# Kernel tuning notes

Measured on AMD Instinct MI355X. Metric: run time of the kernel, lower is better.

The kernel has to match this reference:

```python
import jax, jax.numpy as jnp
import numpy as np

B, N, D, R, H, E = 4, 8192, 16, 32, 64, 262144


def _linear_init(key, fan_in, fan_out):
    return jax.random.normal(key, (fan_in, fan_out), jnp.float32) * (1.0 / np.sqrt(fan_in))


def setup_inputs() -> dict:
    key = jax.random.key(0)
    ks = jax.random.split(key, 8)
    particles = jax.random.normal(ks[0], (B, N, D), jnp.float32)
    senders = jax.random.randint(ks[1], (E,), 0, N, dtype=jnp.int32)
    receivers = jax.random.randint(ks[2], (E,), 0, N, dtype=jnp.int32)
    # relation_encoder: Linear(2D->H), ReLU, Linear(H->R), ReLU
    W1 = _linear_init(ks[3], 2 * D, H)
    b1 = jnp.zeros((H,), jnp.float32)
    W2 = _linear_init(ks[4], H, R)
    b2 = jnp.zeros((R,), jnp.float32)
    # dynamics_fn: Linear(D+R->H), ReLU, Linear(H->D)
    W3 = _linear_init(ks[5], D + R, H)
    b3 = jnp.zeros((H,), jnp.float32)
    W4 = _linear_init(ks[6], H, D)
    b4 = jnp.zeros((D,), jnp.float32)
    return {"particles": particles, "senders": senders, "receivers": receivers,
            "W1": W1, "b1": b1, "W2": W2, "b2": b2,
            "W3": W3, "b3": b3, "W4": W4, "b4": b4}


def reference(particles, senders, receivers, W1, b1, W2, b2, W3, b3, W4, b4):
    # Gather per-edge sender/receiver states: [B, E, D]
    send = particles[:, senders, :]
    recv = particles[:, receivers, :]
    edge_in = jnp.concatenate([send, recv], axis=-1)          # [B, E, 2D]
    # relation_encoder (one batched GEMM over all edges)
    h = jax.nn.relu(edge_in @ W1 + b1)                        # [B, E, H]
    rel_feat = jax.nn.relu(h @ W2 + b2)                       # [B, E, R]
    # scatter-add edge features into receiver nodes
    Bp, Np, _ = particles.shape
    rel = jnp.zeros((Bp, Np, rel_feat.shape[-1]), particles.dtype)
    rel = rel.at[:, receivers, :].add(rel_feat)               # [B, N, R]
    # node update MLP
    dyn_in = jnp.concatenate([particles, rel], axis=-1)       # [B, N, D+R]
    delta = jax.nn.relu(dyn_in @ W3 + b3) @ W4 + b4           # [B, N, D]
    return particles + delta
```

## Files before the change

### kernel.cpp

```cpp
#include <hip/hip_runtime.h>
#include <hip/hip_bf16.h>

namespace {

constexpr int B = 4;
constexpr int N = 8192;
constexpr int D = 16;
constexpr int R = 32;
constexpr int H = 64;
constexpr int E = 262144;

typedef __attribute__((ext_vector_type(8))) short short8;
typedef __attribute__((ext_vector_type(4))) short short4v;
typedef __attribute__((ext_vector_type(4))) float f32x4;

__device__ __forceinline__ float4 ld4(const float* p) {
    return *reinterpret_cast<const float4*>(p);
}
__device__ __forceinline__ float4 fma4(float a, float4 w, float4 c) {
    return float4{fmaf(a, w.x, c.x), fmaf(a, w.y, c.y),
                  fmaf(a, w.z, c.z), fmaf(a, w.w, c.w)};
}
__device__ __forceinline__ float4 relu4(float4 v) {
    return float4{fmaxf(v.x, 0.f), fmaxf(v.y, 0.f), fmaxf(v.z, 0.f), fmaxf(v.w, 0.f)};
}
__device__ __forceinline__ short bf16s(float f) {
    __hip_bfloat16 h = __float2bfloat16(f);
    return __builtin_bit_cast(short, h);
}
__device__ __forceinline__ short8 pack8(float4 a, float4 b) {
    short8 o;
    o[0] = bf16s(a.x); o[1] = bf16s(a.y); o[2] = bf16s(a.z); o[3] = bf16s(a.w);
    o[4] = bf16s(b.x); o[5] = bf16s(b.y); o[6] = bf16s(b.z); o[7] = bf16s(b.w);
    return o;
}
__device__ __forceinline__ short4v pack4_relu(f32x4 c) {
    short4v o;
    o[0] = bf16s(fmaxf(c[0], 0.f)); o[1] = bf16s(fmaxf(c[1], 0.f));
    o[2] = bf16s(fmaxf(c[2], 0.f)); o[3] = bf16s(fmaxf(c[3], 0.f));
    return o;
}
__device__ __forceinline__ float red_get(const int4* uu, int i) {
    const int wsel = i >> 1;
    const int4 v = uu[wsel >> 2];
    const int word = (wsel & 3) == 0 ? v.x : (wsel & 3) == 1 ? v.y
                   : (wsel & 3) == 2 ? v.z : v.w;
    return (i & 1) ? __builtin_bit_cast(float, word & 0xffff0000)
                   : __builtin_bit_cast(float, (unsigned)word << 16);
}

constexpr int RED_S = 264;

__device__ __forceinline__ void prepack_w12(
    int t, const float* __restrict__ W1, const float* __restrict__ W2,
    short* __restrict__ w1p, short* __restrict__ w2p)
{
    for (int i = t; i < 4 * 64 * 8; i += 256) {
        int j = i & 7, lane = (i >> 3) & 63, ct = i >> 9;
        int k = (lane >> 4) * 8 + j, n = ct * 16 + (lane & 15);
        w1p[i] = bf16s(W1[k * H + n]);
    }
    for (int i = t; i < 4 * 64 * 8; i += 256) {
        int j = i & 7, lane = (i >> 3) & 63, idx = i >> 9;
        int ct = idx >> 1, kc = idx & 1;
        int k = kc * 32 + (lane >> 4) * 8 + j, f = ct * 16 + (lane & 15);
        w2p[i] = bf16s(W2[k * R + f]);
    }
}
__device__ __forceinline__ void prepack_w34(
    int t, const float* __restrict__ W3, const float* __restrict__ W4,
    short* __restrict__ w3p, short* __restrict__ w4p)
{
    for (int i = t; i < 8 * 64 * 8; i += 256) {
        int j = i & 7, lane = (i >> 3) & 63, idx = i >> 9;
        int ct = idx >> 1, kc = idx & 1;
        int k = kc * 32 + (lane >> 4) * 8 + j, n = ct * 16 + (lane & 15);
        w3p[i] = (k < D + R) ? bf16s(W3[k * H + n]) : (short)0;
    }
    for (int i = t; i < 2 * 64 * 8; i += 256) {
        int j = i & 7, lane = (i >> 3) & 63, kc = i >> 9;
        int k = kc * 32 + (lane >> 4) * 8 + j, d = lane & 15;
        w4p[i] = bf16s(W4[k * D + d]);
    }
}


__global__ __launch_bounds__(256) void hist_prepack_kernel(
    const int* __restrict__ receivers, int* __restrict__ cnt,
    const float* __restrict__ W1, const float* __restrict__ W2,
    const float* __restrict__ W3, const float* __restrict__ W4,
    short* __restrict__ w1p, short* __restrict__ w2p,
    short* __restrict__ w3p, short* __restrict__ w4p,
    float4* __restrict__ relz)
{
    if (blockIdx.x < 1024) {
        int e = blockIdx.x * 256 + threadIdx.x;
        atomicAdd(cnt + receivers[e], 1);
        return;
    }
    if (blockIdx.x >= 1025) {
        const int base = (blockIdx.x - 1025) * 256 + threadIdx.x;
        #pragma unroll
        for (int i = 0; i < 8; ++i)
            relz[base + i * 32768] = float4{0.f, 0.f, 0.f, 0.f};
        return;
    }
    prepack_w12(threadIdx.x, W1, W2, w1p, w2p);
    prepack_w34(threadIdx.x, W3, W4, w3p, w4p);
}

__global__ __launch_bounds__(1024) void scan_kernel(
    const int* __restrict__ cnt, int* __restrict__ pos)
{
    __shared__ int wtot[16];
    const int t = threadIdx.x;
    const int lane = t & 63;
    int local[8];
    int s = 0;
    #pragma unroll
    for (int i = 0; i < 8; ++i) { local[i] = cnt[t * 8 + i]; s += local[i]; }
    int incl = s;
    #pragma unroll
    for (int d = 1; d < 64; d <<= 1) {
        int v = __shfl_up(incl, d, 64);
        if (lane >= d) incl += v;
    }
    if (lane == 63) wtot[t >> 6] = incl;
    __syncthreads();
    int base = incl - s;
    const int wv = t >> 6;
    #pragma unroll
    for (int i = 0; i < 16; ++i) base += (i < wv) ? wtot[i] : 0;
    #pragma unroll
    for (int i = 0; i < 8; ++i) {
        pos[t * 8 + i] = base;
        base += local[i];
    }
}

__global__ __launch_bounds__(256) void scatter_kernel(
    const int* __restrict__ senders, const int* __restrict__ receivers,
    int* __restrict__ pos, int2* __restrict__ sr)
{
    int e = blockIdx.x * 256 + threadIdx.x;
    if (e < E) {
        int r = receivers[e];
        int p = atomicAdd(pos + r, 1);
        sr[p] = int2{senders[e], r};
    }
}

__global__ __launch_bounds__(256, 4) void edge_mfma_kernel(
    const float* __restrict__ particles,
    const int2*  __restrict__ sr,
    const short* __restrict__ w1p, const float* __restrict__ b1,
    const short* __restrict__ w2p, const float* __restrict__ b2,
    float* __restrict__ rel)
{
    __shared__ short red[R * RED_S];
    __shared__ short hbuf[4][16 * 72];
    __shared__ int   rs[256];

    const int tid  = threadIdx.x;
    const int lane = tid & 63;
    const int w    = tid >> 6;
    const int b    = blockIdx.x >> 10;
    const int p0   = (blockIdx.x & 1023) * 256;
    const int l15  = lane & 15;
    const int q    = lane >> 4;

    const int2 srv = sr[p0 + tid];
    rs[tid] = srv.y;

    float4 a0[4], a1[4];
    #pragma unroll
    for (int t = 0; t < 4; ++t) {
        int srow = __shfl(srv.x, t * 16 + l15);
        int rrow = __shfl(srv.y, t * 16 + l15);
        int row = (q < 2) ? srow : rrow;
        const float* src = particles + ((size_t)b * N + row) * D + (q & 1) * 8;
        a0[t] = ld4(src);
        a1[t] = ld4(src + 4);
    }

    short8 w1f[4], w2f[4];
    #pragma unroll
    for (int mt = 0; mt < 4; ++mt)
        w1f[mt] = *reinterpret_cast<const short8*>(w1p + (mt * 64 + lane) * 8);
    #pragma unroll
    for (int i = 0; i < 4; ++i)
        w2f[i] = *reinterpret_cast<const short8*>(w2p + (i * 64 + lane) * 8);

    f32x4 bias1[4];
    #pragma unroll
    for (int mt = 0; mt < 4; ++mt) {
        float4 t4 = ld4(b1 + mt * 16 + q * 4);
        bias1[mt] = f32x4{t4.x, t4.y, t4.z, t4.w};
    }
    const float bias2a = b2[l15];
    const float bias2b = b2[16 + l15];

    short8 af[4];
    #pragma unroll
    for (int t = 0; t < 4; ++t) af[t] = pack8(a0[t], a1[t]);

    short* hb = &hbuf[w][0];

    #pragma unroll
    for (int t = 0; t < 4; ++t) {
        #pragma unroll
        for (int mt = 0; mt < 4; ++mt) {
            f32x4 c = bias1[mt];
            c = __builtin_amdgcn_mfma_f32_16x16x32_bf16(w1f[mt], af[t], c, 0, 0, 0);
            const int smt = (mt + l15) & 3;
            *reinterpret_cast<short4v*>(hb + l15 * 72 + smt * 16 + q * 4) = pack4_relu(c);
        }
        const int sm0 = ((q >> 1) + l15) & 3;
        const int sm1 = (2 + (q >> 1) + l15) & 3;
        short8 h0 = *reinterpret_cast<const short8*>(hb + l15 * 72 + sm0 * 16 + (q & 1) * 8);
        short8 h1 = *reinterpret_cast<const short8*>(hb + l15 * 72 + sm1 * 16 + (q & 1) * 8);

        f32x4 r0 = {bias2a, bias2a, bias2a, bias2a};
        f32x4 r1 = {bias2b, bias2b, bias2b, bias2b};
        r0 = __builtin_amdgcn_mfma_f32_16x16x32_bf16(h0, w2f[0], r0, 0, 0, 0);
        r0 = __builtin_amdgcn_mfma_f32_16x16x32_bf16(h1, w2f[1], r0, 0, 0, 0);
        r1 = __builtin_amdgcn_mfma_f32_16x16x32_bf16(h0, w2f[2], r1, 0, 0, 0);
        r1 = __builtin_amdgcn_mfma_f32_16x16x32_bf16(h1, w2f[3], r1, 0, 0, 0);

        const int pb2 = w * 64 + t * 16 + q * 4;
        *reinterpret_cast<short4v*>(red + l15 * RED_S + pb2)        = pack4_relu(r0);
        *reinterpret_cast<short4v*>(red + (16 + l15) * RED_S + pb2) = pack4_relu(r1);
    }
    __syncthreads();

    const int g = tid >> 5;
    const int f = tid & 31;
    const int base = g * 32;

    int4 uu[4];
    #pragma unroll
    for (int i = 0; i < 4; ++i)
        uu[i] = *reinterpret_cast<const int4*>(red + f * RED_S + base + 8 * i);
    int4 r4[8];
    #pragma unroll
    for (int i = 0; i < 8; ++i)
        r4[i] = *reinterpret_cast<const int4*>(rs + base + 4 * i);

    const int first = r4[0].x;
    const int last  = r4[7].w;
    if (first == last) {
        float acc = 0.f;
        #pragma unroll
        for (int i = 0; i < 32; ++i) acc += red_get(uu, i);
        atomicAdd(rel + ((size_t)b * N + first) * R + f, acc);
    } else {
        float acc = 0.f;
        int cur = first;
        #pragma unroll
        for (int i = 0; i < 32; ++i) {
            int rr = (i & 3) == 0 ? r4[i >> 2].x : (i & 3) == 1 ? r4[i >> 2].y
                   : (i & 3) == 2 ? r4[i >> 2].z : r4[i >> 2].w;
            float v = red_get(uu, i);
            if (rr != cur) {
                atomicAdd(rel + ((size_t)b * N + cur) * R + f, acc);
                acc = 0.f;
                cur = rr;
            }
            acc += v;
        }
        atomicAdd(rel + ((size_t)b * N + cur) * R + f, acc);
    }
}

__global__ __launch_bounds__(256, 4) void node_mfma_kernel(
    const float* __restrict__ particles,
    const float* __restrict__ rel,
    const short* __restrict__ w3p, const float* __restrict__ b3,
    const short* __restrict__ w4p, const float* __restrict__ b4,
    float* __restrict__ out)
{
    __shared__ short hbuf[4][16 * 72];

    const int tid  = threadIdx.x;
    const int lane = tid & 63;
    const int w    = tid >> 6;
    const int tile = blockIdx.x * 4 + w;
    const int b    = tile >> 9;
    const int l15  = lane & 15;
    const int q    = lane >> 4;
    const int node = (tile & 511) * 16 + l15;

    const float* prow = particles + ((size_t)b * N + node) * D;
    const float* rrow = rel + ((size_t)b * N + node) * R;

    const float* src0 = (q < 2) ? (prow + (q & 1) * 8) : (rrow + (q & 1) * 8);
    float4 c0a = ld4(src0), c0b = ld4(src0 + 4);
    float4 c1a = {0.f, 0.f, 0.f, 0.f}, c1b = {0.f, 0.f, 0.f, 0.f};
    if (q < 2) { c1a = ld4(rrow + 16 + q * 8); c1b = ld4(rrow + 20 + q * 8); }

    short8 w3f[8], w4f[2];
    #pragma unroll
    for (int i = 0; i < 8; ++i)
        w3f[i] = *reinterpret_cast<const short8*>(w3p + (i * 64 + lane) * 8);
    #pragma unroll
    for (int i = 0; i < 2; ++i)
        w4f[i] = *reinterpret_cast<const short8*>(w4p + (i * 64 + lane) * 8);

    f32x4 bias3[4];
    #pragma unroll
    for (int mt = 0; mt < 4; ++mt) {
        float4 t4 = ld4(b3 + mt * 16 + q * 4);
        bias3[mt] = f32x4{t4.x, t4.y, t4.z, t4.w};
    }
    f32x4 bias4;
    { float4 t4 = ld4(b4 + q * 4); bias4 = f32x4{t4.x, t4.y, t4.z, t4.w}; }

    short8 a0 = pack8(c0a, c0b);
    short8 a1 = pack8(c1a, c1b);

    short* hb = &hbuf[w][0];
    #pragma unroll
    for (int mt = 0; mt < 4; ++mt) {
        f32x4 c = bias3[mt];
        c = __builtin_amdgcn_mfma_f32_16x16x32_bf16(w3f[mt * 2 + 0], a0, c, 0, 0, 0);
        c = __builtin_amdgcn_mfma_f32_16x16x32_bf16(w3f[mt * 2 + 1], a1, c, 0, 0, 0);
        *reinterpret_cast<short4v*>(hb + l15 * 72 + mt * 16 + q * 4) = pack4_relu(c);
    }
    short8 h0 = *reinterpret_cast<const short8*>(hb + l15 * 72 + q * 8);
    short8 h1 = *reinterpret_cast<const short8*>(hb + l15 * 72 + 32 + q * 8);

    f32x4 r = bias4;
    r = __builtin_amdgcn_mfma_f32_16x16x32_bf16(w4f[0], h0, r, 0, 0, 0);
    r = __builtin_amdgcn_mfma_f32_16x16x32_bf16(w4f[1], h1, r, 0, 0, 0);

    float4 pv = ld4(prow + q * 4);
    float4* po = reinterpret_cast<float4*>(out + ((size_t)b * N + node) * D + q * 4);
    *po = float4{pv.x + r[0], pv.y + r[1], pv.z + r[2], pv.w + r[3]};
}


__global__ __launch_bounds__(256, 2) void edge_atomic_kernel(
    const float* __restrict__ particles,
    const int*   __restrict__ senders,
    const int*   __restrict__ receivers,
    const float* __restrict__ W1, const float* __restrict__ b1,
    const float* __restrict__ W2, const float* __restrict__ b2,
    float* __restrict__ rel)
{
    const int idx = blockIdx.x * 256 + threadIdx.x;
    const int b = idx >> 18;
    const int e = idx & (E - 1);
    const int s = senders[e];
    const int r = receivers[e];

    float4 ein4[8];
    {
        const float4* ps = reinterpret_cast<const float4*>(particles + ((size_t)b * N + s) * D);
        const float4* pr = reinterpret_cast<const float4*>(particles + ((size_t)b * N + r) * D);
        #pragma unroll
        for (int qq = 0; qq < 4; ++qq) ein4[qq] = ps[qq];
        #pragma unroll
        for (int qq = 0; qq < 4; ++qq) ein4[4 + qq] = pr[qq];
    }
    float4 rf4[8];
    #pragma unroll
    for (int qq = 0; qq < 8; ++qq) rf4[qq] = ld4(b2 + 4 * qq);

    for (int j4 = 0; j4 < H / 4; ++j4) {
        float4 h = ld4(b1 + 4 * j4);
        const float* w1c = W1 + 4 * j4;
        #pragma unroll
        for (int kv = 0; kv < 8; ++kv) {
            const float4 ev = ein4[kv];
            h = fma4(ev.x, ld4(w1c + (4 * kv + 0) * H), h);
            h = fma4(ev.y, ld4(w1c + (4 * kv + 1) * H), h);
            h = fma4(ev.z, ld4(w1c + (4 * kv + 2) * H), h);
            h = fma4(ev.w, ld4(w1c + (4 * kv + 3) * H), h);
        }
        h = relu4(h);
        const float* w2r = W2 + (4 * j4) * R;
        #pragma unroll
        for (int qq = 0; qq < 4; ++qq) {
            const float hq = (qq == 0) ? h.x : (qq == 1) ? h.y : (qq == 2) ? h.z : h.w;
            #pragma unroll
            for (int r4 = 0; r4 < 8; ++r4)
                rf4[r4] = fma4(hq, ld4(w2r + qq * R + 4 * r4), rf4[r4]);
        }
    }
    float* dst = rel + ((size_t)b * N + r) * R;
    #pragma unroll
    for (int r4 = 0; r4 < 8; ++r4) {
        float4 v = relu4(rf4[r4]);
        atomicAdd(dst + 4 * r4 + 0, v.x);
        atomicAdd(dst + 4 * r4 + 1, v.y);
        atomicAdd(dst + 4 * r4 + 2, v.z);
        atomicAdd(dst + 4 * r4 + 3, v.w);
    }
}

__global__ __launch_bounds__(256, 2) void node_valu_kernel(
    const float* __restrict__ particles,
    const float* __restrict__ rel,
    const float* __restrict__ W3, const float* __restrict__ b3,
    const float* __restrict__ W4, const float* __restrict__ b4,
    float* __restrict__ out)
{
    const int idx = blockIdx.x * 256 + threadIdx.x;
    float4 in4[12];
    {
        const float4* pp = reinterpret_cast<const float4*>(particles + (size_t)idx * D);
        #pragma unroll
        for (int qq = 0; qq < 4; ++qq) in4[qq] = pp[qq];
        const float4* pr = reinterpret_cast<const float4*>(rel + (size_t)idx * R);
        #pragma unroll
        for (int qq = 0; qq < 8; ++qq) in4[4 + qq] = pr[qq];
    }
    float4 dl4[4];
    #pragma unroll
    for (int qq = 0; qq < 4; ++qq) dl4[qq] = ld4(b4 + 4 * qq);

    for (int j4 = 0; j4 < H / 4; ++j4) {
        float4 h = ld4(b3 + 4 * j4);
        const float* w3c = W3 + 4 * j4;
        #pragma unroll
        for (int kv = 0; kv < 12; ++kv) {
            const float4 ev = in4[kv];
            h = fma4(ev.x, ld4(w3c + (4 * kv + 0) * H), h);
            h = fma4(ev.y, ld4(w3c + (4 * kv + 1) * H), h);
            h = fma4(ev.z, ld4(w3c + (4 * kv + 2) * H), h);
            h = fma4(ev.w, ld4(w3c + (4 * kv + 3) * H), h);
        }
        h = relu4(h);
        const float* w4r = W4 + (4 * j4) * D;
        #pragma unroll
        for (int qq = 0; qq < 4; ++qq) {
            const float hq = (qq == 0) ? h.x : (qq == 1) ? h.y : (qq == 2) ? h.z : h.w;
            #pragma unroll
            for (int d4 = 0; d4 < 4; ++d4)
                dl4[d4] = fma4(hq, ld4(w4r + qq * D + 4 * d4), dl4[d4]);
        }
    }
    float4* po = reinterpret_cast<float4*>(out + (size_t)idx * D);
    #pragma unroll
    for (int qq = 0; qq < 4; ++qq) {
        float4 v = dl4[qq];
        float4 pv = in4[qq];
        po[qq] = float4{pv.x + v.x, pv.y + v.y, pv.z + v.z, pv.w + v.w};
    }
}

}

extern "C" void kernel_launch(void* const* d_in, const int* in_sizes, int n_in,
                              void* d_out, int out_size, void* d_ws, size_t ws_size,
                              hipStream_t stream) {
    const float* particles = (const float*)d_in[0];
    const int*   senders   = (const int*)d_in[1];
    const int*   receivers = (const int*)d_in[2];
    const float* W1 = (const float*)d_in[3];
    const float* b1 = (const float*)d_in[4];
    const float* W2 = (const float*)d_in[5];
    const float* b2 = (const float*)d_in[6];
    const float* W3 = (const float*)d_in[7];
    const float* b3 = (const float*)d_in[8];
    const float* W4 = (const float*)d_in[9];
    const float* b4 = (const float*)d_in[10];
    float* out = (float*)d_out;

    char* ws = (char*)d_ws;
    size_t off = 0;
    auto take = [&](size_t bytes) -> char* {
        char* p = ws + off;
        off = (off + bytes + 255) & ~(size_t)255;
        return p;
    };
    int*   cnt     = (int*)  take((size_t)N * 4);
    int*   pos     = (int*)  take((size_t)N * 4);
    int2*  sr      = (int2*) take((size_t)E * 8);
    float* rel     = (float*)take((size_t)B * N * R * 4);
    short* w1p     = (short*)take((size_t)4 * 64 * 8 * 2);
    short* w2p     = (short*)take((size_t)4 * 64 * 8 * 2);
    short* w3p     = (short*)take((size_t)8 * 64 * 8 * 2);
    short* w4p     = (short*)take((size_t)2 * 64 * 8 * 2);
    const bool fast = (off <= ws_size);

    if (fast) {
        hipMemsetAsync(cnt, 0, (size_t)N * 4, stream);
        hist_prepack_kernel<<<1153, 256, 0, stream>>>(
            receivers, cnt, W1, W2, W3, W4, w1p, w2p, w3p, w4p, (float4*)rel);
        scan_kernel<<<1, 1024, 0, stream>>>(cnt, pos);
        scatter_kernel<<<E / 256, 256, 0, stream>>>(senders, receivers, pos, sr);
        edge_mfma_kernel<<<(B * E) / 256, 256, 0, stream>>>(
            particles, sr, w1p, b1, w2p, b2, rel);
        node_mfma_kernel<<<(B * N / 16) / 4, 256, 0, stream>>>(
            particles, rel, w3p, b3, w4p, b4, out);
    } else {
        float* rel0 = (float*)d_ws;
        hipMemsetAsync(rel0, 0, (size_t)B * N * R * 4, stream);
        edge_atomic_kernel<<<(B * E) / 256, 256, 0, stream>>>(
            particles, senders, receivers, W1, b1, W2, b2, rel0);
        node_valu_kernel<<<(B * N) / 256, 256, 0, stream>>>(
            particles, rel0, W3, b3, W4, b4, out);
    }
}
```

Before: 136.3 us.

## Loop edge kernel over batches and fold scan into histogram kernel

The edge kernel now handles all four batches in one block. It loads the sorted sender/receiver pairs, the gather offsets, the segment-boundary mask and the packed weights once, and prefetches the next batch's particle rows while computing the current one. The separate single-block scan launch is removed: the last histogram block, found through an atomic done counter, computes the prefix sum. This cuts launch overhead and repeated index and weight loads. The cost is four times fewer edge blocks, extra syncs per batch, and reliance on atomic visibility ordering for the in-kernel scan.

```diff
diff --git a/kernel.cpp b/kernel.cpp
--- a/kernel.cpp
+++ b/kernel.cpp
@@ -84,57 +84,68 @@
     }
 }
 
-
-__global__ __launch_bounds__(256) void hist_prepack_kernel(
+__global__ __launch_bounds__(256) void histscan_prepack_kernel(
     const int* __restrict__ receivers, int* __restrict__ cnt,
+    int* __restrict__ done, int* __restrict__ pos,
     const float* __restrict__ W1, const float* __restrict__ W2,
     const float* __restrict__ W3, const float* __restrict__ W4,
     short* __restrict__ w1p, short* __restrict__ w2p,
     short* __restrict__ w3p, short* __restrict__ w4p,
     float4* __restrict__ relz)
 {
-    if (blockIdx.x < 1024) {
-        int e = blockIdx.x * 256 + threadIdx.x;
-        atomicAdd(cnt + receivers[e], 1);
+    const int tid = threadIdx.x;
+
+    if (blockIdx.x >= 1024) {
+        if (blockIdx.x == 1024) {
+            prepack_w12(tid, W1, W2, w1p, w2p);
+            prepack_w34(tid, W3, W4, w3p, w4p);
+        } else {
+            const int base = (blockIdx.x - 1025) * 256 + tid;
+            #pragma unroll
+            for (int i = 0; i < 8; ++i)
+                relz[base + i * 32768] = float4{0.f, 0.f, 0.f, 0.f};
+        }
         return;
     }
-    if (blockIdx.x >= 1025) {
-        const int base = (blockIdx.x - 1025) * 256 + threadIdx.x;
-        #pragma unroll
-        for (int i = 0; i < 8; ++i)
-            relz[base + i * 32768] = float4{0.f, 0.f, 0.f, 0.f};
-        return;
-    }
-    prepack_w12(threadIdx.x, W1, W2, w1p, w2p);
-    prepack_w34(threadIdx.x, W3, W4, w3p, w4p);
-}
-
-__global__ __launch_bounds__(1024) void scan_kernel(
-    const int* __restrict__ cnt, int* __restrict__ pos)
-{
-    __shared__ int wtot[16];
-    const int t = threadIdx.x;
-    const int lane = t & 63;
-    int local[8];
+
+    atomicAdd(cnt + receivers[blockIdx.x * 256 + tid], 1);
+    __syncthreads();
+
+    __shared__ int amlast;
+    if (tid == 0) {
+        const int old = atomicAdd(done, 1);
+        amlast = (old == 1023) ? 1 : 0;
+    }
+    __syncthreads();
+    if (!amlast) return;
+
+    int c[32];
     int s = 0;
-    #pragma unroll
-    for (int i = 0; i < 8; ++i) { local[i] = cnt[t * 8 + i]; s += local[i]; }
+    const int cb = tid * 32;
+    #pragma unroll
+    for (int i = 0; i < 32; ++i) {
+        c[i] = __hip_atomic_load(cnt + cb + i, __ATOMIC_RELAXED,
+                                 __HIP_MEMORY_SCOPE_AGENT);
+        s += c[i];
+    }
+    const int lane = tid & 63;
+    const int wv   = tid >> 6;
     int incl = s;
     #pragma unroll
     for (int d = 1; d < 64; d <<= 1) {
         int v = __shfl_up(incl, d, 64);
         if (lane >= d) incl += v;
     }
-    if (lane == 63) wtot[t >> 6] = incl;
+    __shared__ int wtot[4];
+    if (lane == 63) wtot[wv] = incl;
     __syncthreads();
     int base = incl - s;
-    const int wv = t >> 6;
-    #pragma unroll
-    for (int i = 0; i < 16; ++i) base += (i < wv) ? wtot[i] : 0;
-    #pragma unroll
-    for (int i = 0; i < 8; ++i) {
-        pos[t * 8 + i] = base;
-        base += local[i];
+    #pragma unroll
+    for (int i = 0; i < 4; ++i) base += (i < wv) ? wtot[i] : 0;
+    #pragma unroll
+    for (int i = 0; i < 32; ++i) {
+        pos[cb + i] = base;
+        base += c[i];
     }
 }
 
@@ -150,7 +161,7 @@
     }
 }
 
-__global__ __launch_bounds__(256, 4) void edge_mfma_kernel(
+__global__ __launch_bounds__(256, 4) void edge_mfma4_kernel(
     const float* __restrict__ particles,
     const int2*  __restrict__ sr,
     const short* __restrict__ w1p, const float* __restrict__ b1,
@@ -164,25 +175,13 @@
     const int tid  = threadIdx.x;
     const int lane = tid & 63;
     const int w    = tid >> 6;
-    const int b    = blockIdx.x >> 10;
-    const int p0   = (blockIdx.x & 1023) * 256;
+    const int p0   = blockIdx.x * 256;
     const int l15  = lane & 15;
     const int q    = lane >> 4;
 
     const int2 srv = sr[p0 + tid];
     rs[tid] = srv.y;
 
-    float4 a0[4], a1[4];
-    #pragma unroll
-    for (int t = 0; t < 4; ++t) {
-        int srow = __shfl(srv.x, t * 16 + l15);
-        int rrow = __shfl(srv.y, t * 16 + l15);
-        int row = (q < 2) ? srow : rrow;
-        const float* src = particles + ((size_t)b * N + row) * D + (q & 1) * 8;
-        a0[t] = ld4(src);
-        a1[t] = ld4(src + 4);
-    }
-
     short8 w1f[4], w2f[4];
     #pragma unroll
     for (int mt = 0; mt < 4; ++mt)
@@ -190,7 +189,6 @@
     #pragma unroll
     for (int i = 0; i < 4; ++i)
         w2f[i] = *reinterpret_cast<const short8*>(w2p + (i * 64 + lane) * 8);
-
     f32x4 bias1[4];
     #pragma unroll
     for (int mt = 0; mt < 4; ++mt) {
@@ -200,75 +198,113 @@
     const float bias2a = b2[l15];
     const float bias2b = b2[16 + l15];
 
-    short8 af[4];
-    #pragma unroll
-    for (int t = 0; t < 4; ++t) af[t] = pack8(a0[t], a1[t]);
+    int off[4];
+    #pragma unroll
+    for (int t = 0; t < 4; ++t) {
+        const int srow = __shfl(srv.x, t * 16 + l15);
+        const int rrow = __shfl(srv.y, t * 16 + l15);
+        off[t] = ((q < 2) ? srow : rrow) * D + (q & 1) * 8;
+    }
+    __syncthreads();
+
+    const int g2 = tid >> 5;
+    const int f  = tid & 31;
+    const int gb = g2 * 32;
+    unsigned bmask = 0;
+    int first;
+    {
+        int4 r4[8];
+        #pragma unroll
+        for (int i = 0; i < 8; ++i)
+            r4[i] = *reinterpret_cast<const int4*>(rs + gb + 4 * i);
+        first = r4[0].x;
+        int prev = first;
+        #pragma unroll
+        for (int i = 1; i < 32; ++i) {
+            const int4 v4 = r4[i >> 2];
+            const int rr = (i & 3) == 0 ? v4.x : (i & 3) == 1 ? v4.y
+                         : (i & 3) == 2 ? v4.z : v4.w;
+            if (rr != prev) bmask |= (1u << i);
+            prev = rr;
+        }
+    }
+
+    float4 g0[4], g1[4];
+    #pragma unroll
+    for (int t = 0; t < 4; ++t) {
+        const float* s0 = particles + off[t];
+        g0[t] = ld4(s0);
+        g1[t] = ld4(s0 + 4);
+    }
 
     short* hb = &hbuf[w][0];
 
-    #pragma unroll
-    for (int t = 0; t < 4; ++t) {
-        #pragma unroll
-        for (int mt = 0; mt < 4; ++mt) {
-            f32x4 c = bias1[mt];
-            c = __builtin_amdgcn_mfma_f32_16x16x32_bf16(w1f[mt], af[t], c, 0, 0, 0);
-            const int smt = (mt + l15) & 3;
-            *reinterpret_cast<short4v*>(hb + l15 * 72 + smt * 16 + q * 4) = pack4_relu(c);
-        }
-        const int sm0 = ((q >> 1) + l15) & 3;
-        const int sm1 = (2 + (q >> 1) + l15) & 3;
-        short8 h0 = *reinterpret_cast<const short8*>(hb + l15 * 72 + sm0 * 16 + (q & 1) * 8);
-        short8 h1 = *reinterpret_cast<const short8*>(hb + l15 * 72 + sm1 * 16 + (q & 1) * 8);
-
-        f32x4 r0 = {bias2a, bias2a, bias2a, bias2a};
-        f32x4 r1 = {bias2b, bias2b, bias2b, bias2b};
-        r0 = __builtin_amdgcn_mfma_f32_16x16x32_bf16(h0, w2f[0], r0, 0, 0, 0);
-        r0 = __builtin_amdgcn_mfma_f32_16x16x32_bf16(h1, w2f[1], r0, 0, 0, 0);
-        r1 = __builtin_amdgcn_mfma_f32_16x16x32_bf16(h0, w2f[2], r1, 0, 0, 0);
-        r1 = __builtin_amdgcn_mfma_f32_16x16x32_bf16(h1, w2f[3], r1, 0, 0, 0);
-
-        const int pb2 = w * 64 + t * 16 + q * 4;
-        *reinterpret_cast<short4v*>(red + l15 * RED_S + pb2)        = pack4_relu(r0);
-        *reinterpret_cast<short4v*>(red + (16 + l15) * RED_S + pb2) = pack4_relu(r1);
-    }
-    __syncthreads();
-
-    const int g = tid >> 5;
-    const int f = tid & 31;
-    const int base = g * 32;
-
-    int4 uu[4];
-    #pragma unroll
-    for (int i = 0; i < 4; ++i)
-        uu[i] = *reinterpret_cast<const int4*>(red + f * RED_S + base + 8 * i);
-    int4 r4[8];
-    #pragma unroll
-    for (int i = 0; i < 8; ++i)
-        r4[i] = *reinterpret_cast<const int4*>(rs + base + 4 * i);
-
-    const int first = r4[0].x;
-    const int last  = r4[7].w;
-    if (first == last) {
-        float acc = 0.f;
-        #pragma unroll
-        for (int i = 0; i < 32; ++i) acc += red_get(uu, i);
-        atomicAdd(rel + ((size_t)b * N + first) * R + f, acc);
-    } else {
-        float acc = 0.f;
-        int cur = first;
-        #pragma unroll
-        for (int i = 0; i < 32; ++i) {
-            int rr = (i & 3) == 0 ? r4[i >> 2].x : (i & 3) == 1 ? r4[i >> 2].y
-                   : (i & 3) == 2 ? r4[i >> 2].z : r4[i >> 2].w;
-            float v = red_get(uu, i);
-            if (rr != cur) {
-                atomicAdd(rel + ((size_t)b * N + cur) * R + f, acc);
-                acc = 0.f;
-                cur = rr;
+    #pragma unroll 1
+    for (int b = 0; b < 4; ++b) {
+        short8 af[4];
+        #pragma unroll
+        for (int t = 0; t < 4; ++t) af[t] = pack8(g0[t], g1[t]);
+        if (b < 3) {
+            const float* nb = particles + (size_t)(b + 1) * N * D;
+            #pragma unroll
+            for (int t = 0; t < 4; ++t) {
+                g0[t] = ld4(nb + off[t]);
+                g1[t] = ld4(nb + off[t] + 4);
             }
-            acc += v;
-        }
-        atomicAdd(rel + ((size_t)b * N + cur) * R + f, acc);
+        }
+
+        #pragma unroll
+        for (int t = 0; t < 4; ++t) {
+            #pragma unroll
+            for (int mt = 0; mt < 4; ++mt) {
+                f32x4 cc = bias1[mt];
+                cc = __builtin_amdgcn_mfma_f32_16x16x32_bf16(w1f[mt], af[t], cc, 0, 0, 0);
+                const int smt = (mt + l15) & 3;
+                *reinterpret_cast<short4v*>(hb + l15 * 72 + smt * 16 + q * 4) = pack4_relu(cc);
+            }
+            const int sm0 = ((q >> 1) + l15) & 3;
+            const int sm1 = (2 + (q >> 1) + l15) & 3;
+            short8 h0 = *reinterpret_cast<const short8*>(hb + l15 * 72 + sm0 * 16 + (q & 1) * 8);
+            short8 h1 = *reinterpret_cast<const short8*>(hb + l15 * 72 + sm1 * 16 + (q & 1) * 8);
+
+            f32x4 r0 = {bias2a, bias2a, bias2a, bias2a};
+            f32x4 r1 = {bias2b, bias2b, bias2b, bias2b};
+            r0 = __builtin_amdgcn_mfma_f32_16x16x32_bf16(h0, w2f[0], r0, 0, 0, 0);
+            r0 = __builtin_amdgcn_mfma_f32_16x16x32_bf16(h1, w2f[1], r0, 0, 0, 0);
+            r1 = __builtin_amdgcn_mfma_f32_16x16x32_bf16(h0, w2f[2], r1, 0, 0, 0);
+            r1 = __builtin_amdgcn_mfma_f32_16x16x32_bf16(h1, w2f[3], r1, 0, 0, 0);
+
+            const int pb2 = w * 64 + t * 16 + q * 4;
+            *reinterpret_cast<short4v*>(red + l15 * RED_S + pb2)        = pack4_relu(r0);
+            *reinterpret_cast<short4v*>(red + (16 + l15) * RED_S + pb2) = pack4_relu(r1);
+        }
+        __syncthreads();
+
+        int4 uu[4];
+        #pragma unroll
+        for (int i = 0; i < 4; ++i)
+            uu[i] = *reinterpret_cast<const int4*>(red + f * RED_S + gb + 8 * i);
+        float* relb = rel + (size_t)b * N * R;
+        if (bmask == 0) {
+            float acc = 0.f;
+            #pragma unroll
+            for (int i = 0; i < 32; ++i) acc += red_get(uu, i);
+            atomicAdd(relb + (size_t)first * R + f, acc);
+        } else {
+            float acc = 0.f;
+            int cur = first;
+            #pragma unroll
+            for (int i = 0; i < 32; ++i) {
+                if (bmask & (1u << i)) {
+                    atomicAdd(relb + (size_t)cur * R + f, acc);
+                    acc = 0.f;
+                    cur = rs[gb + i];
+                }
+                acc += red_get(uu, i);
+            }
+            atomicAdd(relb + (size_t)cur * R + f, acc);
+        }
+        if (b < 3) __syncthreads();
     }
 }
 
@@ -475,6 +511,7 @@
         return p;
     };
     int*   cnt     = (int*)  take((size_t)N * 4);
+    int*   done    = (int*)  take(4);
     int*   pos     = (int*)  take((size_t)N * 4);
     int2*  sr      = (int2*) take((size_t)E * 8);
     float* rel     = (float*)take((size_t)B * N * R * 4);
@@ -485,12 +522,12 @@
     const bool fast = (off <= ws_size);
 
     if (fast) {
-        hipMemsetAsync(cnt, 0, (size_t)N * 4, stream);
-        hist_prepack_kernel<<<1153, 256, 0, stream>>>(
-            receivers, cnt, W1, W2, W3, W4, w1p, w2p, w3p, w4p, (float4*)rel);
-        scan_kernel<<<1, 1024, 0, stream>>>(cnt, pos);
+        hipMemsetAsync(cnt, 0, (size_t)N * 4 + 4, stream);
+        histscan_prepack_kernel<<<1153, 256, 0, stream>>>(
+            receivers, cnt, done, pos,
+            W1, W2, W3, W4, w1p, w2p, w3p, w4p, (float4*)rel);
         scatter_kernel<<<E / 256, 256, 0, stream>>>(senders, receivers, pos, sr);
-        edge_mfma_kernel<<<(B * E) / 256, 256, 0, stream>>>(
+        edge_mfma4_kernel<<<E / 256, 256, 0, stream>>>(
             particles, sr, w1p, b1, w2p, b2, rel);
         node_mfma_kernel<<<(B * N / 16) / 4, 256, 0, stream>>>(
             particles, rel, w3p, b3, w4p, b4, out);
```

After: 207.5 us. +52.3%, slower.
